# Optimization experiments

Measured on AMD Instinct MI355X. Metric: run time of the kernel, lower is better.

## Reference

```python
import jax, jax.numpy as jnp
import numpy as np

THETA = 1.0
V_TH = 1.0       # spikingjelly IFNode default v_threshold
SG_ALPHA = 4.0   # spikingjelly surrogate.Sigmoid default alpha


@jax.custom_vjp
def heaviside(x):
    # spike = 1 if membrane - threshold >= 0
    return (x >= 0).astype(x.dtype)

def _heaviside_fwd(x):
    return (x >= 0).astype(x.dtype), x

def _heaviside_bwd(x, g):
    s = jax.nn.sigmoid(SG_ALPHA * x)
    return (g * SG_ALPHA * s * (1.0 - s),)

heaviside.defvjp(_heaviside_fwd, _heaviside_bwd)


@jax.custom_vjp
def spike_aggregate(spike_out, z_total):
    return spike_out

def _sa_fwd(spike_out, z_total):
    return spike_out, z_total

def _sa_bwd(z_total, g):
    surrogate = (z_total > 0).astype(g.dtype) / THETA
    return (jnp.zeros_like(g), g * surrogate)

spike_aggregate.defvjp(_sa_fwd, _sa_bwd)


def setup_inputs() -> dict:
    key = jax.random.key(0)
    k_x, k_w1, k_b1, k_w2, k_b2 = jax.random.split(key, 5)
    B, D_in, H, D_out = 4096, 784, 800, 10
    x = jax.random.uniform(k_x, (B, D_in), dtype=jnp.float32)
    # nn.Linear-style init: U(-1/sqrt(fan_in), 1/sqrt(fan_in))
    s1 = 1.0 / np.sqrt(D_in)
    s2 = 1.0 / np.sqrt(H)
    W1 = jax.random.uniform(k_w1, (H, D_in), jnp.float32, -s1, s1)
    b1 = jax.random.uniform(k_b1, (H,), jnp.float32, -s1, s1)
    W2 = jax.random.uniform(k_w2, (D_out, H), jnp.float32, -s2, s2)
    b2 = jax.random.uniform(k_b2, (D_out,), jnp.float32, -s2, s2)
    return {"x": x, "W1": W1, "b1": b1, "W2": W2, "b2": b2, "T_sim": 32}


def reference(x, W1, b1, W2, b2, T_sim):
    B = x.shape[0]
    x = x.reshape(B, -1)
    # fixed Bernoulli rate encoding (rand_like(x) < x)
    u = jax.random.uniform(jax.random.key(42), x.shape, dtype=x.dtype)
    x_fixed = (u < x).astype(x.dtype)
    # fc1 input is the same every timestep -> compute once
    cur1 = x_fixed @ W1.T + b1                     # [B, 800]

    def step(carry, _):
        v1, v2, count, z_total = carry
        h1 = v1 + cur1
        spk1 = heaviside(h1 - V_TH)
        v1 = h1 * (1.0 - jax.lax.stop_gradient(spk1))  # hard reset to 0, detach_reset
        cur2 = spk1 @ W2.T + b2                    # [B, 10]
        z_total = z_total + cur2
        h2 = v2 + cur2
        spk2 = heaviside(h2 - V_TH)
        v2 = h2 * (1.0 - jax.lax.stop_gradient(spk2))
        count = count + spk2
        return (v1, v2, count, z_total), None

    H, D_out = W1.shape[0], W2.shape[0]
    init = (jnp.zeros((B, H), x.dtype), jnp.zeros((B, D_out), x.dtype),
            jnp.zeros((B, D_out), x.dtype), jnp.zeros((B, D_out), x.dtype))
    (v1, v2, count, z_total), _ = jax.lax.scan(step, init, None, length=T_sim)
    return spike_aggregate(count, z_total)
```

## Files before the change

kernel.cpp:

```cpp
#include <hip/hip_runtime.h>
#include <stdint.h>

#define B_ROWS 4096
#define D_IN   784
#define H_DIM  800
#define D_OUT  10
#define T_SIM  32
#define N_ELEM (B_ROWS * D_IN)
#define CAP    448

__device__ __forceinline__ void threefry2x32(uint32_t k0, uint32_t k1,
                                             uint32_t& x0, uint32_t& x1) {
  uint32_t ks0 = k0, ks1 = k1, ks2 = k0 ^ k1 ^ 0x1BD11BDAu;
  x0 += ks0; x1 += ks1;
#define TF_RND(r) { x0 += x1; x1 = (x1 << (r)) | (x1 >> (32 - (r))); x1 ^= x0; }
  TF_RND(13) TF_RND(15) TF_RND(26) TF_RND(6)
  x0 += ks1; x1 += ks2 + 1u;
  TF_RND(17) TF_RND(29) TF_RND(16) TF_RND(24)
  x0 += ks2; x1 += ks0 + 2u;
  TF_RND(13) TF_RND(15) TF_RND(26) TF_RND(6)
  x0 += ks0; x1 += ks1 + 3u;
  TF_RND(17) TF_RND(29) TF_RND(16) TF_RND(24)
  x0 += ks1; x1 += ks2 + 4u;
  TF_RND(13) TF_RND(15) TF_RND(26) TF_RND(6)
  x0 += ks2; x1 += ks0 + 5u;
#undef TF_RND
}

__global__ __launch_bounds__(256) void gen_xfixed_T(const float* __restrict__ x,
                                                    float* __restrict__ xfT) {
  const int m = blockIdx.x * 256 + threadIdx.x;
  const int kb = blockIdx.y * 16;
#pragma unroll 1
  for (int kk = 0; kk < 16; ++kk) {
    const int k = kb + kk;
    const int i = m * D_IN + k;
    uint32_t c0 = 0u, c1 = (uint32_t)i;
    threefry2x32(0u, 42u, c0, c1);
    uint32_t bits = c0 ^ c1;
    float u = __uint_as_float((bits >> 9) | 0x3F800000u) - 1.0f;
    xfT[(size_t)k * B_ROWS + m] = (u < x[i]) ? 1.0f : 0.0f;
  }
}

__global__ __launch_bounds__(256) void transpose_w1(const float* __restrict__ W1,
                                                    float* __restrict__ W1T) {
  const int idx = blockIdx.x * 256 + threadIdx.x;
  if (idx >= D_IN * H_DIM) return;
  const int k = idx / H_DIM;
  const int h = idx - k * H_DIM;
  W1T[idx] = W1[h * D_IN + k];
}

#define BK 16

#define GL2LDS(g, l) __builtin_amdgcn_global_load_lds(                      \
    (const __attribute__((address_space(1))) void*)(g),                     \
    (__attribute__((address_space(3))) void*)(l), 16, 0, 0)

__global__ __launch_bounds__(256) void gemm_masks(const float* __restrict__ xfT,
                                                  const float* __restrict__ W1T,
                                                  const float* __restrict__ b1,
                                                  uint32_t* __restrict__ mb) {
  __shared__ __align__(16) float As[2][BK][64];
  __shared__ __align__(16) float Bs[2][BK][64];
  const int t  = threadIdx.x;
  const int tx = t & 15, ty = t >> 4;
  const int m0 = blockIdx.y * 64;
  const int n0 = blockIdx.x * 64;

  const int w = t >> 6;
  const int l = t & 63;
  const int skk = 4 * w + (l >> 4);
  const int sm  = (l & 15) * 4;
  const float* gA = xfT + (size_t)skk * B_ROWS + m0 + sm;
  const float* gB = W1T + (size_t)skk * H_DIM + n0 + sm;

#define STAGE(buf, tt) {                                                    \
    GL2LDS(gA + (size_t)(tt) * BK * B_ROWS, &As[buf][4 * w][0]);            \
    GL2LDS(gB + (size_t)(tt) * BK * H_DIM,  &Bs[buf][4 * w][0]); }

  STAGE(0, 0);
  __syncthreads();

  float acc[4][4] = {};
  const int NT = D_IN / BK;
#pragma unroll 1
  for (int tt = 0; tt < NT; ++tt) {
    const int cur = tt & 1;
    if (tt + 1 < NT) STAGE(cur ^ 1, tt + 1);
#pragma unroll
    for (int kk = 0; kk < BK; kk++) {
      float4 av = *(const float4*)&As[cur][kk][ty * 4];
      float4 bv = *(const float4*)&Bs[cur][kk][tx * 4];
      float a[4] = {av.x, av.y, av.z, av.w};
      float b[4] = {bv.x, bv.y, bv.z, bv.w};
#pragma unroll
      for (int mi = 0; mi < 4; mi++)
#pragma unroll
        for (int ni = 0; ni < 4; ni++)
          acc[mi][ni] = __builtin_fmaf(a[mi], b[ni], acc[mi][ni]);
    }
    __syncthreads();
  }
#undef STAGE

  const int hOut = n0 + tx * 4;
  if (hOut < H_DIM) {
    float4 bb = *(const float4*)&b1[hOut];
#pragma unroll
    for (int mi = 0; mi < 4; mi++) {
      int m = m0 + ty * 4 + mi;
      float c4[4] = {acc[mi][0] + bb.x, acc[mi][1] + bb.y,
                     acc[mi][2] + bb.z, acc[mi][3] + bb.w};
      uint32_t mk4[4];
#pragma unroll
      for (int ni = 0; ni < 4; ni++) {
        float c = c4[ni];
        float v = 0.0f;
        int p = 0;
#pragma unroll 1
        for (int s = 1; s <= T_SIM; s++) {
          float h1 = v + c;
          if (h1 >= 1.0f) { p = s; break; }
          v = h1;
        }
        uint32_t mk = 0;
        if (p) for (int s = p; s <= T_SIM; s += p) mk |= 1u << (s - 1);
        mk4[ni] = mk;
      }
      *(uint4*)&mb[(size_t)m * H_DIM + hOut] =
          make_uint4(mk4[0], mk4[1], mk4[2], mk4[3]);
    }
  }
}

__global__ __launch_bounds__(320) void snn_scan(const uint32_t* __restrict__ mb,
                                                const float* __restrict__ W2,
                                                const float* __restrict__ b2,
                                                float* __restrict__ out) {
  __shared__ __align__(16) float W2T[H_DIM * D_OUT];
  __shared__ __align__(16) uint2 pkS[2][CAP];
  __shared__ int   lenS[2];
  __shared__ float b2f[D_OUT];
  float* c2s = (float*)&pkS[0][0];
  const int tid  = threadIdx.x;
  const int row0 = blockIdx.x * 2;

  if (tid < D_OUT) b2f[tid] = b2[tid];

  if (tid < 128) {
    const int r = tid >> 6, ln = tid & 63;
    const uint64_t lm = (1ull << ln) - 1ull;
    const uint32_t* mrow = mb + (size_t)(row0 + r) * H_DIM;
    uint32_t mv[13];
#pragma unroll
    for (int ch = 0; ch < 13; ++ch) {
      int h = ch * 64 + ln;
      mv[ch] = (h < H_DIM) ? mrow[h] : 0u;
    }
    int off = 0;
#pragma unroll
    for (int ch = 0; ch < 13; ++ch) {
      bool g = (mv[ch] != 0u);
      uint64_t bal = __ballot(g);
      int pos = off + __popcll(bal & lm);
      if (g && pos < CAP) {
        uint2 pk; pk.x = (uint32_t)((ch * 64 + ln) * 40); pk.y = mv[ch];
        pkS[r][pos] = pk;
      }
      off += __popcll(bal);
    }
    if (off <= CAP) {
      int lp = (off + 63) & ~63;
      int i = off + ln;
      if (i < lp) { pkS[r][i].x = 0u; pkS[r][i].y = 0u; }
    }
    if (ln == 0) lenS[r] = off;
  } else {
    for (int e = tid - 128; e < H_DIM * D_OUT; e += 192) {
      int o = e / H_DIM, h = e - o * H_DIM;
      W2T[h * D_OUT + o] = W2[e];
    }
  }
  __syncthreads();

  float s0 = 0.0f, s1 = 0.0f;
  const int j = tid >> 6;
  const int lane = tid & 63;
  const int t = lane & 31;
  const int r = lane >> 5;
  const bool ovf = (lenS[0] > CAP) || (lenS[1] > CAP);
  {
    if (!ovf) {
      const int Lpad = (lenS[r] + 63) & ~63;
      const uint2* pp = pkS[r];
      const char* wbase = (const char*)W2T + 8 * j;
#pragma unroll 8
      for (int i = 0; i < Lpad; ++i) {
        uint2 pk = pp[i];
        float2 w = *(const float2*)(wbase + pk.x);
        bool g = (pk.y >> t) & 1u;
        s0 += g ? w.x : 0.0f;
        s1 += g ? w.y : 0.0f;
      }
    } else {
      const uint32_t* mrow = mb + (size_t)(row0 + r) * H_DIM;
      const uint32_t vbit = 1u << t;
      for (int h = 0; h < H_DIM; ++h) {
        uint32_t mk = mrow[h];
        float2 w = *(const float2*)&W2T[h * D_OUT + 2 * j];
        s0 += (mk & vbit) ? w.x : 0.0f;
        s1 += (mk & vbit) ? w.y : 0.0f;
      }
    }
  }
  __syncthreads();
  c2s[((r * T_SIM) + t) * D_OUT + 2 * j]     = s0;
  c2s[((r * T_SIM) + t) * D_OUT + 2 * j + 1] = s1;
  __syncthreads();

  if (tid < 2 * D_OUT) {
    const int rr = tid / D_OUT, o = tid % D_OUT;
    const float bb = b2f[o];
    float v = 0.0f; int cnt = 0;
#pragma unroll
    for (int tt = 0; tt < T_SIM; ++tt) {
      float cur2 = c2s[((rr * T_SIM) + tt) * D_OUT + o] + bb;
      float h2 = v + cur2;
      bool spk = (h2 >= 1.0f);
      cnt += spk ? 1 : 0;
      v = spk ? 0.0f : h2;
    }
    out[(size_t)(row0 + rr) * D_OUT + o] = (float)cnt;
  }
}

extern "C" void kernel_launch(void* const* d_in, const int* in_sizes, int n_in,
                              void* d_out, int out_size, void* d_ws, size_t ws_size,
                              hipStream_t stream) {
  const float* x  = (const float*)d_in[0];
  const float* W1 = (const float*)d_in[1];
  const float* b1 = (const float*)d_in[2];
  const float* W2 = (const float*)d_in[3];
  const float* b2 = (const float*)d_in[4];
  float* outp = (float*)d_out;

  float*    xfT  = (float*)d_ws;
  float*    W1T  = xfT + (size_t)D_IN * B_ROWS;
  uint32_t* mbuf = (uint32_t*)(W1T + (size_t)D_IN * H_DIM);

  gen_xfixed_T<<<dim3(16, 49), 256, 0, stream>>>(x, xfT);
  transpose_w1<<<(D_IN * H_DIM + 255) / 256, 256, 0, stream>>>(W1, W1T);

  dim3 g1(13, 64);
  gemm_masks<<<g1, 256, 0, stream>>>(xfT, W1T, b1, mbuf);

  snn_scan<<<B_ROWS / 2, 320, 0, stream>>>(mbuf, W2, b2, outp);
}
```

Baseline: 280.1 us.

## Triple-buffer GEMM LDS staging with prefetch distance two and explicit waitcnts

Moves the fc1 GEMM's global-to-LDS staging from double to triple buffering, prefetching two tiles ahead. Each iteration now waits with an explicit vmcnt and a raw s_barrier instead of a full __syncthreads, so more load latency can overlap compute. This costs more LDS per block and relies on hand-counted waitcnt values. A miscount could cause data races, and the second-to-last iteration appears to wait with vmcnt(2) even though no new load was issued.

Result: slower. 317.3 us (+13.3%).

```diff
diff --git a/kernel.cpp b/kernel.cpp
--- a/kernel.cpp
+++ b/kernel.cpp
@@ -62,8 +62,8 @@
                                                   const float* __restrict__ W1T,
                                                   const float* __restrict__ b1,
                                                   uint32_t* __restrict__ mb) {
-  __shared__ __align__(16) float As[2][BK][64];
-  __shared__ __align__(16) float Bs[2][BK][64];
+  __shared__ __align__(16) float As[3][BK][64];
+  __shared__ __align__(16) float Bs[3][BK][64];
   const int t  = threadIdx.x;
   const int tx = t & 15, ty = t >> 4;
   const int m0 = blockIdx.y * 64;
@@ -80,30 +80,44 @@
     GL2LDS(gA + (size_t)(tt) * BK * B_ROWS, &As[buf][4 * w][0]);            \
     GL2LDS(gB + (size_t)(tt) * BK * H_DIM,  &Bs[buf][4 * w][0]); }
 
-  STAGE(0, 0);
-  __syncthreads();
+#define COMPUTE(buf) {                                                      \
+    _Pragma("unroll")                                                       \
+    for (int kk = 0; kk < BK; kk++) {                                       \
+      float4 av = *(const float4*)&As[buf][kk][ty * 4];                     \
+      float4 bv = *(const float4*)&Bs[buf][kk][tx * 4];                     \
+      float a[4] = {av.x, av.y, av.z, av.w};                                \
+      float b[4] = {bv.x, bv.y, bv.z, bv.w};                                \
+      _Pragma("unroll")                                                     \
+      for (int mi = 0; mi < 4; mi++)                                        \
+        _Pragma("unroll")                                                   \
+        for (int ni = 0; ni < 4; ni++)                                      \
+          acc[mi][ni] = __builtin_fmaf(a[mi], b[ni], acc[mi][ni]);          \
+    } }
 
   float acc[4][4] = {};
   const int NT = D_IN / BK;
+
+  STAGE(0, 0);
+  STAGE(1, 1);
+
+  int cur = 0;
 #pragma unroll 1
-  for (int tt = 0; tt < NT; ++tt) {
-    const int cur = tt & 1;
-    if (tt + 1 < NT) STAGE(cur ^ 1, tt + 1);
-#pragma unroll
-    for (int kk = 0; kk < BK; kk++) {
-      float4 av = *(const float4*)&As[cur][kk][ty * 4];
-      float4 bv = *(const float4*)&Bs[cur][kk][tx * 4];
-      float a[4] = {av.x, av.y, av.z, av.w};
-      float b[4] = {bv.x, bv.y, bv.z, bv.w};
-#pragma unroll
-      for (int mi = 0; mi < 4; mi++)
-#pragma unroll
-        for (int ni = 0; ni < 4; ni++)
-          acc[mi][ni] = __builtin_fmaf(a[mi], b[ni], acc[mi][ni]);
-    }
-    __syncthreads();
-  }
+  for (int tt = 0; tt < NT - 1; ++tt) {
+    asm volatile("s_waitcnt vmcnt(2)" ::: "memory");
+    __builtin_amdgcn_s_barrier();
+    if (tt + 2 < NT) {
+      int sb = cur + 2; if (sb >= 3) sb -= 3;
+      STAGE(sb, tt + 2);
+    }
+    COMPUTE(cur);
+    asm volatile("s_waitcnt lgkmcnt(0)" ::: "memory");
+    cur = cur + 1; if (cur >= 3) cur = 0;
+  }
+  asm volatile("s_waitcnt vmcnt(0)" ::: "memory");
+  __builtin_amdgcn_s_barrier();
+  COMPUTE(cur);
 #undef STAGE
+#undef COMPUTE
 
   const int hOut = n0 + tx * 4;
   if (hOut < H_DIM) {
```

## Enlarge GEMM M-tile to 128 and read pre-transposed W2 from global

Applied to the files above, without the earlier changes.

The mask GEMM now computes a 128x64 tile per block with 8x4 accumulators per thread, which halves the grid and improves A/B reuse per LDS load. A separate small kernel pre-transposes W2 into global memory, and snn_scan now reads weights from global/L2 instead of building a 32 KB LDS copy in every block. This removes the per-block W2 transpose and frees LDS for occupancy, at the cost of gathered global loads in the inner accumulation loop and fewer GEMM blocks (416) across the GPU.

Result: slower. 389.3 us (+39.0%).

```diff
diff --git a/kernel.cpp b/kernel.cpp
--- a/kernel.cpp
+++ b/kernel.cpp
@@ -52,6 +52,15 @@
   W1T[idx] = W1[h * D_IN + k];
 }
 
+__global__ __launch_bounds__(256) void transpose_w2(const float* __restrict__ W2,
+                                                    float* __restrict__ W2GT) {
+  const int idx = blockIdx.x * 256 + threadIdx.x;
+  if (idx >= H_DIM * D_OUT) return;
+  const int h = idx / D_OUT;
+  const int o = idx - h * D_OUT;
+  W2GT[idx] = W2[o * H_DIM + h];
+}
+
 #define BK 16
 
 #define GL2LDS(g, l) __builtin_amdgcn_global_load_lds(                      \
@@ -62,28 +71,34 @@
                                                   const float* __restrict__ W1T,
                                                   const float* __restrict__ b1,
                                                   uint32_t* __restrict__ mb) {
-  __shared__ __align__(16) float As[2][BK][64];
+  __shared__ __align__(16) float As[2][BK][128];
   __shared__ __align__(16) float Bs[2][BK][64];
   const int t  = threadIdx.x;
-  const int tx = t & 15, ty = t >> 4;
-  const int m0 = blockIdx.y * 64;
+  const int tx = t & 15;
+  const int ty = t >> 4;
+  const int m0 = blockIdx.y * 128;
   const int n0 = blockIdx.x * 64;
 
   const int w = t >> 6;
   const int l = t & 63;
-  const int skk = 4 * w + (l >> 4);
-  const int sm  = (l & 15) * 4;
-  const float* gA = xfT + (size_t)skk * B_ROWS + m0 + sm;
-  const float* gB = W1T + (size_t)skk * H_DIM + n0 + sm;
+  const int skkA0 = 4 * w + 0 + (l >> 5);
+  const int skkA1 = 4 * w + 2 + (l >> 5);
+  const int smA   = (l & 31) * 4;
+  const int skkB  = 4 * w + (l >> 4);
+  const int smB   = (l & 15) * 4;
+  const float* gA0 = xfT + (size_t)skkA0 * B_ROWS + m0 + smA;
+  const float* gA1 = xfT + (size_t)skkA1 * B_ROWS + m0 + smA;
+  const float* gB  = W1T + (size_t)skkB * H_DIM + n0 + smB;
 
 #define STAGE(buf, tt) {                                                    \
-    GL2LDS(gA + (size_t)(tt) * BK * B_ROWS, &As[buf][4 * w][0]);            \
-    GL2LDS(gB + (size_t)(tt) * BK * H_DIM,  &Bs[buf][4 * w][0]); }
+    GL2LDS(gA0 + (size_t)(tt) * BK * B_ROWS, &As[buf][4 * w][0]);           \
+    GL2LDS(gA1 + (size_t)(tt) * BK * B_ROWS, &As[buf][4 * w + 2][0]);       \
+    GL2LDS(gB  + (size_t)(tt) * BK * H_DIM,  &Bs[buf][4 * w][0]); }
 
   STAGE(0, 0);
   __syncthreads();
 
-  float acc[4][4] = {};
+  float acc[8][4] = {};
   const int NT = D_IN / BK;
 #pragma unroll 1
   for (int tt = 0; tt < NT; ++tt) {
@@ -91,12 +106,13 @@
     if (tt + 1 < NT) STAGE(cur ^ 1, tt + 1);
 #pragma unroll
     for (int kk = 0; kk < BK; kk++) {
-      float4 av = *(const float4*)&As[cur][kk][ty * 4];
-      float4 bv = *(const float4*)&Bs[cur][kk][tx * 4];
-      float a[4] = {av.x, av.y, av.z, av.w};
+      float4 av0 = *(const float4*)&As[cur][kk][ty * 8];
+      float4 av1 = *(const float4*)&As[cur][kk][ty * 8 + 4];
+      float4 bv  = *(const float4*)&Bs[cur][kk][tx * 4];
+      float a[8] = {av0.x, av0.y, av0.z, av0.w, av1.x, av1.y, av1.z, av1.w};
       float b[4] = {bv.x, bv.y, bv.z, bv.w};
 #pragma unroll
-      for (int mi = 0; mi < 4; mi++)
+      for (int mi = 0; mi < 8; mi++)
 #pragma unroll
         for (int ni = 0; ni < 4; ni++)
           acc[mi][ni] = __builtin_fmaf(a[mi], b[ni], acc[mi][ni]);
@@ -109,8 +125,8 @@
   if (hOut < H_DIM) {
     float4 bb = *(const float4*)&b1[hOut];
 #pragma unroll
-    for (int mi = 0; mi < 4; mi++) {
-      int m = m0 + ty * 4 + mi;
+    for (int mi = 0; mi < 8; mi++) {
+      int m = m0 + ty * 8 + mi;
       float c4[4] = {acc[mi][0] + bb.x, acc[mi][1] + bb.y,
                      acc[mi][2] + bb.z, acc[mi][3] + bb.w};
       uint32_t mk4[4];
@@ -136,10 +152,9 @@
 }
 
 __global__ __launch_bounds__(320) void snn_scan(const uint32_t* __restrict__ mb,
-                                                const float* __restrict__ W2,
+                                                const float* __restrict__ W2GT,
                                                 const float* __restrict__ b2,
                                                 float* __restrict__ out) {
-  __shared__ __align__(16) float W2T[H_DIM * D_OUT];
   __shared__ __align__(16) uint2 pkS[2][CAP];
   __shared__ int   lenS[2];
   __shared__ float b2f[D_OUT];
@@ -177,11 +192,6 @@
       if (i < lp) { pkS[r][i].x = 0u; pkS[r][i].y = 0u; }
     }
     if (ln == 0) lenS[r] = off;
-  } else {
-    for (int e = tid - 128; e < H_DIM * D_OUT; e += 192) {
-      int o = e / H_DIM, h = e - o * H_DIM;
-      W2T[h * D_OUT + o] = W2[e];
-    }
   }
   __syncthreads();
 
@@ -192,14 +202,14 @@
   const int r = lane >> 5;
   const bool ovf = (lenS[0] > CAP) || (lenS[1] > CAP);
   {
+    const char* wg = (const char*)W2GT + 8 * j;
     if (!ovf) {
       const int Lpad = (lenS[r] + 63) & ~63;
       const uint2* pp = pkS[r];
-      const char* wbase = (const char*)W2T + 8 * j;
 #pragma unroll 8
       for (int i = 0; i < Lpad; ++i) {
         uint2 pk = pp[i];
-        float2 w = *(const float2*)(wbase + pk.x);
+        float2 w = *(const float2*)(wg + pk.x);
         bool g = (pk.y >> t) & 1u;
         s0 += g ? w.x : 0.0f;
         s1 += g ? w.y : 0.0f;
@@ -209,7 +219,7 @@
       const uint32_t vbit = 1u << t;
       for (int h = 0; h < H_DIM; ++h) {
         uint32_t mk = mrow[h];
-        float2 w = *(const float2*)&W2T[h * D_OUT + 2 * j];
+        float2 w = *(const float2*)(wg + h * 40);
         s0 += (mk & vbit) ? w.x : 0.0f;
         s1 += (mk & vbit) ? w.y : 0.0f;
       }
@@ -248,13 +258,15 @@
 
   float*    xfT  = (float*)d_ws;
   float*    W1T  = xfT + (size_t)D_IN * B_ROWS;
-  uint32_t* mbuf = (uint32_t*)(W1T + (size_t)D_IN * H_DIM);
+  float*    W2GT = W1T + (size_t)D_IN * H_DIM;
+  uint32_t* mbuf = (uint32_t*)(W2GT + H_DIM * D_OUT);
 
   gen_xfixed_T<<<dim3(16, 49), 256, 0, stream>>>(x, xfT);
   transpose_w1<<<(D_IN * H_DIM + 255) / 256, 256, 0, stream>>>(W1, W1T);
-
-  dim3 g1(13, 64);
+  transpose_w2<<<(H_DIM * D_OUT + 255) / 256, 256, 0, stream>>>(W2, W2GT);
+
+  dim3 g1(13, 32);
   gemm_masks<<<g1, 256, 0, stream>>>(xfT, W1T, b1, mbuf);
 
-  snn_scan<<<B_ROWS / 2, 320, 0, stream>>>(mbuf, W2, b2, outp);
-}
+  snn_scan<<<B_ROWS / 2, 320, 0, stream>>>(mbuf, W2GT, b2, outp);
+}
```
